# Optimization experiments

Hardware: AMD Instinct MI355X
Metric: run time of the kernel (lower is better)

## Reference

```python
import jax, jax.numpy as jnp
import numpy as np

B, D, E, H, F, V = 65536, 8, 16, 80, 9, 100000
IN = E * (F + 1)  # 160


def setup_inputs() -> dict:
    key = jax.random.key(0)
    ks = jax.random.split(key, 14)
    pid = jax.random.randint(ks[0], (B,), 0, D + 1)            # 0 = padding, 1..D = domains
    feats = jax.random.randint(ks[1], (B, F), 0, V)
    emb_pid = (jax.random.normal(ks[2], (D + 1, E), jnp.float32) * 0.1).at[0].set(0.0)
    emb_feats = (jax.random.normal(ks[3], (F, V + 1, E), jnp.float32) * 0.1).at[:, 0, :].set(0.0)
    shared_w1 = jax.random.normal(ks[4], (IN, H), jnp.float32) * 0.1
    dom_w1 = jax.random.normal(ks[5], (D, IN, H), jnp.float32) * 0.1
    shared_b1 = jax.random.normal(ks[6], (H,), jnp.float32) * 0.1
    dom_b1 = jax.random.normal(ks[7], (D, H), jnp.float32) * 0.1
    shared_w2 = jax.random.normal(ks[8], (H,), jnp.float32) * 0.1
    dom_w2 = jax.random.normal(ks[9], (D, H), jnp.float32) * 0.1
    shared_b2 = jax.random.normal(ks[10], (), jnp.float32) * 0.1
    dom_b2 = jax.random.normal(ks[11], (D,), jnp.float32) * 0.1
    dl_w = jax.random.normal(ks[12], (E,), jnp.float32) * 0.1
    dl_b = jax.random.normal(ks[13], (), jnp.float32) * 0.1
    return {"pid": pid, "feats": feats, "emb_pid": emb_pid, "emb_feats": emb_feats,
            "shared_w1": shared_w1, "dom_w1": dom_w1, "shared_b1": shared_b1, "dom_b1": dom_b1,
            "shared_w2": shared_w2, "dom_w2": dom_w2, "shared_b2": shared_b2, "dom_b2": dom_b2,
            "dl_w": dl_w, "dl_b": dl_b}


def reference(pid, feats, emb_pid, emb_feats, shared_w1, dom_w1, shared_b1, dom_b1,
              shared_w2, dom_w2, shared_b2, dom_b2, dl_w, dl_b):
    # embedding lookup + relu (dropout is identity at inference)
    e_pid = jax.nn.relu(emb_pid[pid])                          # (B, E)
    e_f = jax.nn.relu(emb_feats[jnp.arange(F), feats])         # (B, F, E)
    out = jnp.concatenate([e_pid, e_f.reshape(B, F * E)], axis=-1)  # (B, IN)
    # star-merge: elementwise product of shared and per-domain kernels, additive biases
    W1 = shared_w1[None] * dom_w1                              # (D, IN, H)
    b1 = shared_b1[None] + dom_b1                              # (D, H)
    h = jax.nn.relu(jnp.einsum('bi,dih->dbh', out, W1) + b1[:, None, :])  # (D, B, H)
    W2 = shared_w2[None] * dom_w2                              # (D, H)
    b2 = shared_b2 + dom_b2                                    # (D,)
    l = jnp.einsum('dbh,dh->db', h, W2) + b2[:, None]          # (D, B)
    # scatter-combine: each sample takes its own domain's logit (0 for padding pid)
    sel = pid[None, :] == (jnp.arange(D) + 1)[:, None]         # (D, B)
    logits = jnp.sum(jnp.where(sel, l, 0.0), axis=0)           # (B,)
    domain_logits = e_pid @ dl_w + dl_b                        # (B,)
    return logits + domain_logits
```

## Files before the change

kernel.cpp:

```cpp
#include <hip/hip_runtime.h>
#include <hip/hip_bf16.h>

#define NB 65536
#define ND 8
#define NE 16
#define NH 80
#define NF 9
#define NV 100000
#define NIN 160
#define WND 1024
#define NWND (NB / WND)

typedef __attribute__((ext_vector_type(8))) short short8;
typedef __attribute__((ext_vector_type(4))) float float4v;

__device__ inline unsigned short f2bf(float x) {
  unsigned int u = __float_as_uint(x);
  return (unsigned short)((u + 0x7fffu + ((u >> 16) & 1u)) >> 16);
}
__device__ inline unsigned int cvt2(float x, float y) {
  union { __hip_bfloat162 h; unsigned int u; } cv;
  cv.h = __float22bfloat162_rn(make_float2(x, y));
  return cv.u;
}

__global__ __launch_bounds__(512, 4) void k_main(
    const int* __restrict__ pid, const int* __restrict__ feats,
    const float* __restrict__ emb_pid, const float* __restrict__ emb_feats,
    const float* __restrict__ sw1, const float* __restrict__ dw1,
    const float* __restrict__ sb1, const float* __restrict__ db1,
    const float* __restrict__ sw2, const float* __restrict__ dw2,
    const float* __restrict__ sb2, const float* __restrict__ db2,
    const float* __restrict__ dl_w, const float* __restrict__ dl_b,
    float* __restrict__ out) {
  const int d = blockIdx.x >> 6;
  const int wnd = blockIdx.x & 63;
  const int t = threadIdx.x, wave = t >> 6, lane = t & 63;

  __shared__ unsigned short sA[128][168];
  __shared__ unsigned short sBF[5][5][4][16][8];
  __shared__ int sOrig[WND];
  __shared__ int cnt0[8], cnt1[8];

  const int b0 = wnd * WND + t;
  const int b1 = b0 + 512;
  const int p0 = pid[b0];
  const int p1 = pid[b1];

  for (int i = t; i < NIN * NH; i += 512) {
    int k = i / NH, n = i % NH;
    float w = sw1[i] * dw1[d * (NIN * NH) + i];
    sBF[n >> 4][k >> 5][(k >> 3) & 3][n & 15][k & 7] = f2bf(w);
  }

  const float dlb = dl_b[0];
  float dlacc = dlb;
  unsigned int ep[8];
  {
    const float* __restrict__ row = emb_pid + (d + 1) * NE;
#pragma unroll
    for (int i = 0; i < NE; i += 2) {
      float x0 = fmaxf(row[i], 0.f), x1 = fmaxf(row[i + 1], 0.f);
      dlacc = fmaf(x0, dl_w[i], dlacc);
      dlacc = fmaf(x1, dl_w[i + 1], dlacc);
      ep[i >> 1] = cvt2(x0, x1);
    }
  }
  float b1l[5], w2l[5];
#pragma unroll
  for (int nt = 0; nt < 5; ++nt) {
    int h = nt * 16 + (lane & 15);
    b1l[nt] = sb1[h] + db1[d * NH + h];
    w2l[nt] = sw2[h] * dw2[d * NH + h];
  }
  const float b2 = sb2[0] + db2[d];

  if (d == 0) {
    if (p0 == 0) out[b0] = dlb;
    if (p1 == 0) out[b1] = dlb;
  }

  unsigned long long m0 = __ballot(p0 == d + 1);
  unsigned long long m1 = __ballot(p1 == d + 1);
  if (lane == 0) { cnt0[wave] = (int)__popcll(m0); cnt1[wave] = (int)__popcll(m1); }
  const unsigned long long lt = (1ull << lane) - 1ull;
  const int r0 = (int)__popcll(m0 & lt);
  const int r1 = (int)__popcll(m1 & lt);
  __syncthreads();
  int base0 = 0, tot0 = 0, base1 = 0, tot1 = 0;
#pragma unroll
  for (int w = 0; w < 8; ++w) {
    if (w < wave) { base0 += cnt0[w]; base1 += cnt1[w]; }
    tot0 += cnt0[w]; tot1 += cnt1[w];
  }
  const int c = tot0 + tot1;
  if (p0 == d + 1) sOrig[base0 + r0] = b0;
  if (p1 == d + 1) sOrig[tot0 + base1 + r1] = b1;
  __syncthreads();

  for (int g0 = 0; g0 < c; g0 += 128) {
    const int s = t >> 2, q = t & 3;
    int ss = g0 + s; if (ss >= c) ss = c - 1;
    const int bb = sOrig[ss];

    int idx[NF];
#pragma unroll
    for (int f = 0; f < NF; ++f) idx[f] = feats[bb * NF + f];
    float4 vv[NF];
#pragma unroll
    for (int f = 0; f < NF; ++f)
      vv[f] = *(const float4*)(emb_feats +
                               (size_t)((f * (NV + 1) + idx[f]) * NE + q * 4));
    if (q < 2) {
      unsigned int* dst = (unsigned int*)&sA[s][0];
#pragma unroll
      for (int j = 0; j < 4; ++j) dst[q * 4 + j] = ep[q * 4 + j];
    }
#pragma unroll
    for (int f = 0; f < NF; ++f) {
      unsigned int lo = cvt2(fmaxf(vv[f].x, 0.f), fmaxf(vv[f].y, 0.f));
      unsigned int hi = cvt2(fmaxf(vv[f].z, 0.f), fmaxf(vv[f].w, 0.f));
      unsigned int* dst = (unsigned int*)&sA[s][16 + f * 16];
      dst[q * 2] = lo;
      dst[q * 2 + 1] = hi;
    }
    __syncthreads();

    float4v acc[5];
#pragma unroll
    for (int nt = 0; nt < 5; ++nt)
      acc[nt] = (float4v){b1l[nt], b1l[nt], b1l[nt], b1l[nt]};
    const int arow = wave * 16 + (lane & 15);
    const int koff = (lane >> 4) * 8;
#pragma unroll
    for (int ks = 0; ks < 5; ++ks) {
      short8 af = *(const short8*)&sA[arow][ks * 32 + koff];
#pragma unroll
      for (int nt = 0; nt < 5; ++nt) {
        short8 bf = *(const short8*)&sBF[nt][ks][lane >> 4][lane & 15][0];
        acc[nt] = __builtin_amdgcn_mfma_f32_16x16x32_bf16(af, bf, acc[nt], 0, 0, 0);
      }
    }

    float pr[4];
#pragma unroll
    for (int r = 0; r < 4; ++r) {
      float a2 = 0.f;
#pragma unroll
      for (int nt = 0; nt < 5; ++nt) a2 = fmaf(fmaxf(acc[nt][r], 0.f), w2l[nt], a2);
      pr[r] = a2;
    }
#pragma unroll
    for (int r = 0; r < 4; ++r) {
      pr[r] += __shfl_xor(pr[r], 1);
      pr[r] += __shfl_xor(pr[r], 2);
      pr[r] += __shfl_xor(pr[r], 4);
      pr[r] += __shfl_xor(pr[r], 8);
    }
    if ((lane & 15) == 0) {
      int srow2 = wave * 16 + (lane >> 4) * 4;
#pragma unroll
      for (int r = 0; r < 4; ++r) {
        int kk = g0 + srow2 + r;
        if (kk < c) out[sOrig[kk]] = pr[r] + b2 + dlacc;
      }
    }
    if (g0 + 128 < c) __syncthreads();
  }
}

extern "C" void kernel_launch(void* const* d_in, const int* in_sizes, int n_in,
                              void* d_out, int out_size, void* d_ws, size_t ws_size,
                              hipStream_t stream) {
  const int*   pid      = (const int*)d_in[0];
  const int*   feats    = (const int*)d_in[1];
  const float* emb_pid  = (const float*)d_in[2];
  const float* emb_f    = (const float*)d_in[3];
  const float* sw1      = (const float*)d_in[4];
  const float* dw1      = (const float*)d_in[5];
  const float* sb1      = (const float*)d_in[6];
  const float* db1      = (const float*)d_in[7];
  const float* sw2      = (const float*)d_in[8];
  const float* dw2      = (const float*)d_in[9];
  const float* sb2      = (const float*)d_in[10];
  const float* db2      = (const float*)d_in[11];
  const float* dl_w     = (const float*)d_in[12];
  const float* dl_b     = (const float*)d_in[13];
  float* out = (float*)d_out;
  (void)d_ws; (void)ws_size;

  k_main<<<NWND * ND, 512, 0, stream>>>(pid, feats, emb_pid, emb_f, sw1, dw1,
                                        sb1, db1, sw2, dw2, sb2, db2, dl_w,
                                        dl_b, out);
}
```

Baseline: 26.87 us.

## Warp-specialize producer/consumer waves with double-buffered LDS tiles

Splits the block into four producer waves that gather and convert embedding rows into one LDS buffer while four consumer waves run the MFMA GEMM and output on the other buffer. Tiles shrink from 128 to 64 rows so that gather latency overlaps compute. The cost is that each phase now uses only half the waves. With about 114 rows per block there are only about two tiles, so the prologue is exposed and there is little to overlap.

```diff
diff --git a/kernel.cpp b/kernel.cpp
--- a/kernel.cpp
+++ b/kernel.cpp
@@ -37,7 +37,7 @@
   const int wnd = blockIdx.x & 63;
   const int t = threadIdx.x, wave = t >> 6, lane = t & 63;
 
-  __shared__ unsigned short sA[128][168];
+  __shared__ unsigned short sA[2][64][168];
   __shared__ unsigned short sBF[5][5][4][16][8];
   __shared__ int sOrig[WND];
   __shared__ int cnt0[8], cnt1[8];
@@ -87,22 +87,27 @@
   const int r0 = (int)__popcll(m0 & lt);
   const int r1 = (int)__popcll(m1 & lt);
   __syncthreads();
-  int base0 = 0, tot0 = 0, base1 = 0, tot1 = 0;
+  int base0 = 0, tot0 = 0, base1 = 0;
 #pragma unroll
   for (int w = 0; w < 8; ++w) {
     if (w < wave) { base0 += cnt0[w]; base1 += cnt1[w]; }
-    tot0 += cnt0[w]; tot1 += cnt1[w];
-  }
-  const int c = tot0 + tot1;
+    tot0 += cnt0[w];
+  }
+  int c = tot0;
+#pragma unroll
+  for (int w = 0; w < 8; ++w) c += cnt1[w];
   if (p0 == d + 1) sOrig[base0 + r0] = b0;
   if (p1 == d + 1) sOrig[tot0 + base1 + r1] = b1;
   __syncthreads();
 
-  for (int g0 = 0; g0 < c; g0 += 128) {
-    const int s = t >> 2, q = t & 3;
+  if (c == 0) return;
+  const int ntiles = (c + 63) >> 6;
+  const bool prod = wave >= 4;
+
+  auto stage = [&](int buf, int g0) {
+    const int s = (t & 255) >> 2, q = t & 3;
     int ss = g0 + s; if (ss >= c) ss = c - 1;
     const int bb = sOrig[ss];
-
     int idx[NF];
 #pragma unroll
     for (int f = 0; f < NF; ++f) idx[f] = feats[bb * NF + f];
@@ -112,7 +117,7 @@
       vv[f] = *(const float4*)(emb_feats +
                                (size_t)((f * (NV + 1) + idx[f]) * NE + q * 4));
     if (q < 2) {
-      unsigned int* dst = (unsigned int*)&sA[s][0];
+      unsigned int* dst = (unsigned int*)&sA[buf][s][0];
 #pragma unroll
       for (int j = 0; j < 4; ++j) dst[q * 4 + j] = ep[q * 4 + j];
     }
@@ -120,52 +125,61 @@
     for (int f = 0; f < NF; ++f) {
       unsigned int lo = cvt2(fmaxf(vv[f].x, 0.f), fmaxf(vv[f].y, 0.f));
       unsigned int hi = cvt2(fmaxf(vv[f].z, 0.f), fmaxf(vv[f].w, 0.f));
-      unsigned int* dst = (unsigned int*)&sA[s][16 + f * 16];
+      unsigned int* dst = (unsigned int*)&sA[buf][s][16 + f * 16];
       dst[q * 2] = lo;
       dst[q * 2 + 1] = hi;
     }
+  };
+
+  if (prod) stage(0, 0);
+  __syncthreads();
+
+  for (int k = 0; k < ntiles; ++k) {
+    const int g0 = k * 64;
+    if (prod) {
+      if (k + 1 < ntiles) stage((k + 1) & 1, g0 + 64);
+    } else if (g0 + wave * 16 < c) {
+      const int buf = k & 1;
+      float4v acc[5];
+#pragma unroll
+      for (int nt = 0; nt < 5; ++nt)
+        acc[nt] = (float4v){b1l[nt], b1l[nt], b1l[nt], b1l[nt]};
+      const int arow = wave * 16 + (lane & 15);
+      const int koff = (lane >> 4) * 8;
+#pragma unroll
+      for (int ks = 0; ks < 5; ++ks) {
+        short8 af = *(const short8*)&sA[buf][arow][ks * 32 + koff];
+#pragma unroll
+        for (int nt = 0; nt < 5; ++nt) {
+          short8 bf = *(const short8*)&sBF[nt][ks][lane >> 4][lane & 15][0];
+          acc[nt] = __builtin_amdgcn_mfma_f32_16x16x32_bf16(af, bf, acc[nt], 0, 0, 0);
+        }
+      }
+      float pr[4];
+#pragma unroll
+      for (int r = 0; r < 4; ++r) {
+        float a2 = 0.f;
+#pragma unroll
+        for (int nt = 0; nt < 5; ++nt) a2 = fmaf(fmaxf(acc[nt][r], 0.f), w2l[nt], a2);
+        pr[r] = a2;
+      }
+#pragma unroll
+      for (int r = 0; r < 4; ++r) {
+        pr[r] += __shfl_xor(pr[r], 1);
+        pr[r] += __shfl_xor(pr[r], 2);
+        pr[r] += __shfl_xor(pr[r], 4);
+        pr[r] += __shfl_xor(pr[r], 8);
+      }
+      if ((lane & 15) == 0) {
+        int srow2 = wave * 16 + (lane >> 4) * 4;
+#pragma unroll
+        for (int r = 0; r < 4; ++r) {
+          int kk = g0 + srow2 + r;
+          if (kk < c) out[sOrig[kk]] = pr[r] + b2 + dlacc;
+        }
+      }
+    }
     __syncthreads();
-
-    float4v acc[5];
-#pragma unroll
-    for (int nt = 0; nt < 5; ++nt)
-      acc[nt] = (float4v){b1l[nt], b1l[nt], b1l[nt], b1l[nt]};
-    const int arow = wave * 16 + (lane & 15);
-    const int koff = (lane >> 4) * 8;
-#pragma unroll
-    for (int ks = 0; ks < 5; ++ks) {
-      short8 af = *(const short8*)&sA[arow][ks * 32 + koff];
-#pragma unroll
-      for (int nt = 0; nt < 5; ++nt) {
-        short8 bf = *(const short8*)&sBF[nt][ks][lane >> 4][lane & 15][0];
-        acc[nt] = __builtin_amdgcn_mfma_f32_16x16x32_bf16(af, bf, acc[nt], 0, 0, 0);
-      }
-    }
-
-    float pr[4];
-#pragma unroll
-    for (int r = 0; r < 4; ++r) {
-      float a2 = 0.f;
-#pragma unroll
-      for (int nt = 0; nt < 5; ++nt) a2 = fmaf(fmaxf(acc[nt][r], 0.f), w2l[nt], a2);
-      pr[r] = a2;
-    }
-#pragma unroll
-    for (int r = 0; r < 4; ++r) {
-      pr[r] += __shfl_xor(pr[r], 1);
-      pr[r] += __shfl_xor(pr[r], 2);
-      pr[r] += __shfl_xor(pr[r], 4);
-      pr[r] += __shfl_xor(pr[r], 8);
-    }
-    if ((lane & 15) == 0) {
-      int srow2 = wave * 16 + (lane >> 4) * 4;
-#pragma unroll
-      for (int r = 0; r < 4; ++r) {
-        int kk = g0 + srow2 + r;
-        if (kk < c) out[sOrig[kk]] = pr[r] + b2 + dlacc;
-      }
-    }
-    if (g0 + 128 < c) __syncthreads();
   }
 }
 
```

After: 24.60 us. -8.5%, faster.
